# Performance work log

Measured on AMD Instinct MI355X. Metric: run time of the kernel, lower is better.

## Reference

```python
import jax, jax.numpy as jnp
import numpy as np

IN_SIZE = 4096   # input_size
OUT_SIZE = 4096  # output_size
RANK = 1024      # len(S_4), multiple of 32
GROUPSIZE = 128
BITS = 4
PACK = 32 // BITS  # 8 nibbles per int32
MAXQ_MASK = (1 << BITS) - 1  # 15


def _dequant4(qweight, qzeros, scales, g_idx):
    """GPTQ 4-bit dequant. qweight: int32 [K//8, N]; qzeros: int32 [G, N//8];
    scales: [G, N]; g_idx: int32 [K]. Returns W [K, N] with
    W[k, n] = (int4[k, n] - (zero4[g_idx[k], n] + 1)) * scales[g_idx[k], n]."""
    shifts = (jnp.arange(PACK, dtype=jnp.int32) * BITS)
    K = qweight.shape[0] * PACK
    N = qweight.shape[1]
    # unpack along rows: [K//8, 8, N] -> [K, N]
    intw = ((qweight[:, None, :] >> shifts[None, :, None]) & MAXQ_MASK).reshape(K, N)
    # unpack along cols: [G, N//8, 8] -> [G, N]; pack() stored zeros-1, so add 1 back
    zeros = ((qzeros[:, :, None] >> shifts[None, None, :]) & MAXQ_MASK).reshape(qzeros.shape[0], N) + 1
    sc = scales[g_idx]            # [K, N]
    zr = zeros[g_idx].astype(scales.dtype)  # [K, N]
    return (intw.astype(scales.dtype) - zr) * sc


def setup_inputs() -> dict:
    key = jax.random.key(0)
    ks = jax.random.split(key, 9)
    qweight_V = jax.random.randint(ks[0], (IN_SIZE // PACK, RANK), 0, 2**31 - 1, dtype=jnp.int32)
    qzeros_V = jax.random.randint(ks[1], (IN_SIZE // GROUPSIZE, RANK // PACK), 0, 2**31 - 1, dtype=jnp.int32)
    scales_V = jax.random.uniform(ks[2], (IN_SIZE // GROUPSIZE, RANK), dtype=jnp.float32) * 0.01 + 1e-3
    g_idx_V = (jnp.arange(IN_SIZE, dtype=jnp.int32) // GROUPSIZE).astype(jnp.int32)
    qweight_U = jax.random.randint(ks[3], (RANK // PACK, OUT_SIZE), 0, 2**31 - 1, dtype=jnp.int32)
    qzeros_U = jax.random.randint(ks[4], (RANK // GROUPSIZE, OUT_SIZE // PACK), 0, 2**31 - 1, dtype=jnp.int32)
    scales_U = jax.random.uniform(ks[5], (RANK // GROUPSIZE, OUT_SIZE), dtype=jnp.float32) * 0.01 + 1e-3
    g_idx_U = (jnp.arange(RANK, dtype=jnp.int32) // GROUPSIZE).astype(jnp.int32)
    S = jax.random.uniform(ks[6], (RANK,), dtype=jnp.float32) + 0.1  # singular values
    x = jax.random.normal(ks[7], (4, 2048, IN_SIZE), dtype=jnp.float32)
    return {"x": x,
            "qweight_V": qweight_V, "qzeros_V": qzeros_V, "scales_V": scales_V, "g_idx_V": g_idx_V,
            "qweight_U": qweight_U, "qzeros_U": qzeros_U, "scales_U": scales_U, "g_idx_U": g_idx_U,
            "S": S}


def reference(x, qweight_V, qzeros_V, scales_V, g_idx_V,
              qweight_U, qzeros_U, scales_U, g_idx_U, S):
    # weight_V: dequantized [IN_SIZE, RANK]; weight_U: dequantized [RANK, OUT_SIZE]
    weight_V = _dequant4(qweight_V, qzeros_V, scales_V, g_idx_V)
    weight_U = _dequant4(qweight_U, qzeros_U, scales_U, g_idx_U)
    # forward returns (weight_V @ diag(S) @ weight_U).T  -> [OUT_SIZE, IN_SIZE]
    # (the x @ W_V @ diag(S) @ W_U activation path in the source is dead code
    #  w.r.t. the returned value)
    return ((weight_V * S[None, :]) @ weight_U).T
```

## Files before the change

kernel.cpp:

```cpp
#include <hip/hip_runtime.h>

typedef __attribute__((ext_vector_type(8))) short bf16x8;
typedef __attribute__((ext_vector_type(4))) float f32x4;

__device__ __forceinline__ short f2bf(float f) {
  unsigned u = __builtin_bit_cast(unsigned, f);
  u += 0x7fffu + ((u >> 16) & 1u);
  return (short)(u >> 16);
}


__global__ __launch_bounds__(256) void dequant_v(const int* __restrict__ qw,
                                                 const int* __restrict__ qz,
                                                 const float* __restrict__ sc,
                                                 const float* __restrict__ S,
                                                 short* __restrict__ P) {
  const int t  = blockIdx.x * 256 + threadIdx.x;
  const int r8 = t & 127;
  const int k  = t >> 7;
  const int g  = k >> 7;
  const int kw = k >> 3;
  const int sh = (k & 7) << 2;
  const int r0 = r8 << 3;
  const int zw = qz[(g << 7) + r8];
  const int*   wq  = qw + kw * 1024 + r0;
  const float* scp = sc + (g << 10) + r0;
  const float* sp  = S + r0;
  bf16x8 res;
#pragma unroll
  for (int i = 0; i < 8; ++i) {
    int q = (wq[i] >> sh) & 15;
    int z = ((zw >> (i << 2)) & 15) + 1;
    res[i] = f2bf((float)(q - z) * scp[i] * sp[i]);
  }
  *(bf16x8*)(P + (k << 10) + r0) = res;
}

__global__ __launch_bounds__(256) void dequant_u(const int* __restrict__ qw,
                                                 const int* __restrict__ qz,
                                                 const float* __restrict__ sc,
                                                 short* __restrict__ Qt) {
  const int t  = blockIdx.x * 256 + threadIdx.x;
  const int rw = t & 127;
  const int n  = t >> 7;
  const int g  = rw >> 4;
  const int w  = qw[(rw << 12) + n];
  const int zw = qz[(g << 9) + (n >> 3)];
  const int z  = ((zw >> ((n & 7) << 2)) & 15) + 1;
  const float s = sc[(g << 12) + n];
  bf16x8 res;
#pragma unroll
  for (int i = 0; i < 8; ++i) {
    int q = (w >> (i << 2)) & 15;
    res[i] = f2bf((float)(q - z) * s);
  }
  *(bf16x8*)(Qt + (n << 10) + (rw << 3)) = res;
}

#define GLL(g, l)                                                              \
  __builtin_amdgcn_global_load_lds(                                            \
      (const __attribute__((address_space(1))) void*)(g),                      \
      (__attribute__((address_space(3))) void*)(l), 16, 0, 0)

__global__ __launch_bounds__(512, 2) void gemm256(const short* __restrict__ P,
                                                  const short* __restrict__ Qt,
                                                  float* __restrict__ out) {
  __shared__ __align__(16) char lds[131072];
  const int tid  = threadIdx.x;
  const int lane = tid & 63;
  const int wid  = tid >> 6;
  const int wm   = wid >> 2;
  const int wn   = wid & 3;
  const int m0 = (blockIdx.x >> 4) << 8;
  const int n0 = (blockIdx.x & 15) << 8;

  const int srow = tid >> 3;
  const int scol = ((tid & 7) << 4) ^ ((srow & 7) << 4);
  const short* gA = P  + (m0 + srow) * 1024 + (scol >> 1);
  const short* gB = Qt + (n0 + srow) * 1024 + (scol >> 1);

#define STG(gp, roff, half, ktv) do {                                          \
    const short* s_ = (gp) + (half) * 131072 + ((ktv) << 6);                   \
    char* d_ = lds + (roff) + (half) * 16384 + (wid << 10);                    \
    GLL(s_, d_);                                                               \
    GLL(s_ + 65536, d_ + 8192);                                                \
  } while (0)

  const int arow_b = ((wm << 7) + (lane & 15)) << 7;
  const int brow_b = ((wn << 6) + (lane & 15)) << 7;
  const int klo  = (lane >> 4) << 4;
  const int swz  = (lane & 7) << 4;
  const int offk0 = klo ^ swz;
  const int offk1 = (klo | 64) ^ swz;

  f32x4 acc[8][4];
#pragma unroll
  for (int mi = 0; mi < 8; ++mi)
#pragma unroll
    for (int ni = 0; ni < 4; ++ni) acc[mi][ni] = f32x4{0.f, 0.f, 0.f, 0.f};

  bf16x8 ah[4][2], bh0[2][2], bh1[2][2];

  STG(gA, 0, 0, 0);
  STG(gA, 0, 1, 0);
  STG(gB, 32768, 0, 0);
  STG(gB, 32768, 1, 0);
  STG(gA, 65536, 0, 1);
  STG(gA, 65536, 1, 1);
  STG(gB, 65536 + 32768, 0, 1);
  STG(gB, 65536 + 32768, 1, 1);
  asm volatile("s_waitcnt vmcnt(8)" ::: "memory");
  __builtin_amdgcn_s_barrier();

  for (int kt = 0; kt < 16; ++kt) {
    const int curbuf = (kt & 1) << 16;
    const char* Ab = lds + curbuf;
    const char* Bb = Ab + 32768;

#pragma unroll
    for (int i = 0; i < 4; ++i) {
      ah[i][0] = *(const bf16x8*)(Ab + arow_b + i * 2048 + offk0);
      ah[i][1] = *(const bf16x8*)(Ab + arow_b + i * 2048 + offk1);
    }
#pragma unroll
    for (int j = 0; j < 2; ++j) {
      bh0[j][0] = *(const bf16x8*)(Bb + brow_b + j * 2048 + offk0);
      bh0[j][1] = *(const bf16x8*)(Bb + brow_b + j * 2048 + offk1);
    }
    asm volatile("s_waitcnt lgkmcnt(0)" ::: "memory");
    __builtin_amdgcn_sched_barrier(0);
    __builtin_amdgcn_s_setprio(1);
#pragma unroll
    for (int kk = 0; kk < 2; ++kk)
#pragma unroll
      for (int i = 0; i < 4; ++i)
#pragma unroll
        for (int j = 0; j < 2; ++j)
          acc[i][j] = __builtin_amdgcn_mfma_f32_16x16x32_bf16(
              ah[i][kk], bh0[j][kk], acc[i][j], 0, 0, 0);
    __builtin_amdgcn_s_setprio(0);
    __builtin_amdgcn_s_barrier();

#pragma unroll
    for (int j = 0; j < 2; ++j) {
      bh1[j][0] = *(const bf16x8*)(Bb + brow_b + 4096 + j * 2048 + offk0);
      bh1[j][1] = *(const bf16x8*)(Bb + brow_b + 4096 + j * 2048 + offk1);
    }
    asm volatile("s_waitcnt lgkmcnt(0)" ::: "memory");
    __builtin_amdgcn_sched_barrier(0);
    __builtin_amdgcn_s_setprio(1);
#pragma unroll
    for (int kk = 0; kk < 2; ++kk)
#pragma unroll
      for (int i = 0; i < 4; ++i)
#pragma unroll
        for (int j = 0; j < 2; ++j)
          acc[i][2 + j] = __builtin_amdgcn_mfma_f32_16x16x32_bf16(
              ah[i][kk], bh1[j][kk], acc[i][2 + j], 0, 0, 0);
    __builtin_amdgcn_s_setprio(0);
    __builtin_amdgcn_s_barrier();

#pragma unroll
    for (int i = 0; i < 4; ++i) {
      ah[i][0] = *(const bf16x8*)(Ab + arow_b + 8192 + i * 2048 + offk0);
      ah[i][1] = *(const bf16x8*)(Ab + arow_b + 8192 + i * 2048 + offk1);
    }
    if (kt < 14) {
      STG(gB, curbuf + 32768, 0, kt + 2);
      STG(gB, curbuf + 32768, 1, kt + 2);
    }
    asm volatile("s_waitcnt lgkmcnt(0)" ::: "memory");
    __builtin_amdgcn_sched_barrier(0);
    __builtin_amdgcn_s_setprio(1);
#pragma unroll
    for (int kk = 0; kk < 2; ++kk)
#pragma unroll
      for (int i = 0; i < 4; ++i)
#pragma unroll
        for (int j = 0; j < 2; ++j)
          acc[4 + i][2 + j] = __builtin_amdgcn_mfma_f32_16x16x32_bf16(
              ah[i][kk], bh1[j][kk], acc[4 + i][2 + j], 0, 0, 0);
    __builtin_amdgcn_s_setprio(0);
    __builtin_amdgcn_s_barrier();

    if (kt < 14) {
      STG(gA, curbuf, 0, kt + 2);
      STG(gA, curbuf, 1, kt + 2);
    }
    __builtin_amdgcn_s_setprio(1);
#pragma unroll
    for (int kk = 0; kk < 2; ++kk)
#pragma unroll
      for (int i = 0; i < 4; ++i)
#pragma unroll
        for (int j = 0; j < 2; ++j)
          acc[4 + i][j] = __builtin_amdgcn_mfma_f32_16x16x32_bf16(
              ah[i][kk], bh0[j][kk], acc[4 + i][j], 0, 0, 0);
    __builtin_amdgcn_s_setprio(0);
    if (kt == 14) asm volatile("s_waitcnt vmcnt(0)" ::: "memory");
    else          asm volatile("s_waitcnt vmcnt(8)" ::: "memory");
    __builtin_amdgcn_s_barrier();
  }

  const int mbase = m0 + (wm << 7) + ((lane >> 4) << 2);
  const int nbase = n0 + (wn << 6) + (lane & 15);
#pragma unroll
  for (int mi = 0; mi < 8; ++mi)
#pragma unroll
    for (int ni = 0; ni < 4; ++ni)
      *(f32x4*)(out + (size_t)(nbase + ni * 16) * 4096 + mbase + mi * 16) =
          acc[mi][ni];
#undef STG
}

extern "C" void kernel_launch(void* const* d_in, const int* in_sizes, int n_in,
                              void* d_out, int out_size, void* d_ws, size_t ws_size,
                              hipStream_t stream) {
  const int*   qw_V = (const int*)d_in[1];
  const int*   qz_V = (const int*)d_in[2];
  const float* sc_V = (const float*)d_in[3];
  const int*   qw_U = (const int*)d_in[5];
  const int*   qz_U = (const int*)d_in[6];
  const float* sc_U = (const float*)d_in[7];
  const float* S    = (const float*)d_in[9];

  short* P  = (short*)d_ws;
  short* Qt = (short*)d_ws + 4096 * 1024;
  float* out = (float*)d_out;

  dequant_v<<<2048, 256, 0, stream>>>(qw_V, qz_V, sc_V, S, P);
  dequant_u<<<2048, 256, 0, stream>>>(qw_U, qz_U, sc_U, Qt);
  gemm256<<<256, 512, 0, stream>>>(P, Qt, out);
}
```

Measured before the change: 55.05 us.

## Pre-tile dequantized operands into MFMA fragment order for contiguous LDS staging

The dequant kernels now write A and B in a tile-major layout that matches the per-lane MFMA fragment order, so each 256x64 K-tile is a contiguous 32KB chunk. The GEMM stages it with contiguous global_load_lds copies and reads LDS at lane-linear offsets, dropping the XOR swizzle and per-row address math. The aim is fully coalesced global loads and conflict-free LDS reads. In exchange, the dequant kernels' reads are less coalesced, especially the V weight gathers.

```diff
diff --git a/kernel.cpp b/kernel.cpp
--- a/kernel.cpp
+++ b/kernel.cpp
@@ -14,47 +14,55 @@
                                                  const int* __restrict__ qz,
                                                  const float* __restrict__ sc,
                                                  const float* __restrict__ S,
-                                                 short* __restrict__ P) {
-  const int t  = blockIdx.x * 256 + threadIdx.x;
-  const int r8 = t & 127;
-  const int k  = t >> 7;
-  const int g  = k >> 7;
-  const int kw = k >> 3;
-  const int sh = (k & 7) << 2;
-  const int r0 = r8 << 3;
-  const int zw = qz[(g << 7) + r8];
-  const int*   wq  = qw + kw * 1024 + r0;
+                                                 short* __restrict__ A) {
+  const int t    = blockIdx.x * 256 + threadIdx.x;
+  const int tile = t >> 11;
+  const int blk  = (t >> 6) & 31;
+  const int lane = t & 63;
+  const int panel = tile >> 4, kt = tile & 15;
+  const int m  = (panel << 8) + (((blk >> 4) & 1) << 7) + (((blk >> 1) & 7) << 4) + (lane & 15);
+  const int r0 = (kt << 6) + ((blk & 1) << 5) + ((lane >> 4) << 3);
+
+  const int g  = m >> 7;
+  const int sh = (m & 7) << 2;
+  const int zw = qz[(g << 7) + (r0 >> 3)];
+  const int*   wq  = qw + (m >> 3) * 1024 + r0;
   const float* scp = sc + (g << 10) + r0;
   const float* sp  = S + r0;
   bf16x8 res;
 #pragma unroll
-  for (int i = 0; i < 8; ++i) {
-    int q = (wq[i] >> sh) & 15;
-    int z = ((zw >> (i << 2)) & 15) + 1;
-    res[i] = f2bf((float)(q - z) * scp[i] * sp[i]);
+  for (int e = 0; e < 8; ++e) {
+    int q = (wq[e] >> sh) & 15;
+    int z = ((zw >> (e << 2)) & 15) + 1;
+    res[e] = f2bf((float)(q - z) * scp[e] * sp[e]);
   }
-  *(bf16x8*)(P + (k << 10) + r0) = res;
+  *(bf16x8*)(A + ((size_t)t << 3)) = res;
 }
 
 __global__ __launch_bounds__(256) void dequant_u(const int* __restrict__ qw,
                                                  const int* __restrict__ qz,
                                                  const float* __restrict__ sc,
-                                                 short* __restrict__ Qt) {
-  const int t  = blockIdx.x * 256 + threadIdx.x;
-  const int rw = t & 127;
-  const int n  = t >> 7;
-  const int g  = rw >> 4;
-  const int w  = qw[(rw << 12) + n];
+                                                 short* __restrict__ B) {
+  const int t    = blockIdx.x * 256 + threadIdx.x;
+  const int tile = t >> 11;
+  const int blk  = (t >> 6) & 31;
+  const int lane = t & 63;
+  const int panel = tile >> 4, kt = tile & 15;
+  const int n  = (panel << 8) + (((blk >> 3) & 3) << 6) + (((blk >> 1) & 3) << 4) + (lane & 15);
+  const int r0 = (kt << 6) + ((blk & 1) << 5) + ((lane >> 4) << 3);
+
+  const int w  = qw[(r0 >> 3) * 4096 + n];
+  const int g  = r0 >> 7;
   const int zw = qz[(g << 9) + (n >> 3)];
   const int z  = ((zw >> ((n & 7) << 2)) & 15) + 1;
   const float s = sc[(g << 12) + n];
   bf16x8 res;
 #pragma unroll
-  for (int i = 0; i < 8; ++i) {
-    int q = (w >> (i << 2)) & 15;
-    res[i] = f2bf((float)(q - z) * s);
+  for (int e = 0; e < 8; ++e) {
+    int q = (w >> (e << 2)) & 15;
+    res[e] = f2bf((float)(q - z) * s);
   }
-  *(bf16x8*)(Qt + (n << 10) + (rw << 3)) = res;
+  *(bf16x8*)(B + ((size_t)t << 3)) = res;
 }
 
 #define GLL(g, l)                                                              \
@@ -62,8 +70,8 @@
       (const __attribute__((address_space(1))) void*)(g),                      \
       (__attribute__((address_space(3))) void*)(l), 16, 0, 0)
 
-__global__ __launch_bounds__(512, 2) void gemm256(const short* __restrict__ P,
-                                                  const short* __restrict__ Qt,
+__global__ __launch_bounds__(512, 2) void gemm256(const short* __restrict__ A,
+                                                  const short* __restrict__ B,
                                                   float* __restrict__ out) {
   __shared__ __align__(16) char lds[131072];
   const int tid  = threadIdx.x;
@@ -71,27 +79,31 @@
   const int wid  = tid >> 6;
   const int wm   = wid >> 2;
   const int wn   = wid & 3;
-  const int m0 = (blockIdx.x >> 4) << 8;
-  const int n0 = (blockIdx.x & 15) << 8;
-
-  const int srow = tid >> 3;
-  const int scol = ((tid & 7) << 4) ^ ((srow & 7) << 4);
-  const short* gA = P  + (m0 + srow) * 1024 + (scol >> 1);
-  const short* gB = Qt + (n0 + srow) * 1024 + (scol >> 1);
-
-#define STG(gp, roff, half, ktv) do {                                          \
-    const short* s_ = (gp) + (half) * 131072 + ((ktv) << 6);                   \
-    char* d_ = lds + (roff) + (half) * 16384 + (wid << 10);                    \
-    GLL(s_, d_);                                                               \
-    GLL(s_ + 65536, d_ + 8192);                                                \
+  const int mp = blockIdx.x >> 4;
+  const int np = blockIdx.x & 15;
+
+  const short* gA = A + ((size_t)(mp * 16) << 14) + (wid << 11) + (lane << 3);
+  const short* gB = B + ((size_t)(np * 16) << 14) + (wid << 11) + (lane << 3);
+
+#define STGA(buf, ktv) do {                                                    \
+    const short* s_ = gA + ((ktv) << 14);                                      \
+    char* d_ = lds + (buf) + (wid << 12);                                      \
+    GLL(s_,        d_);                                                        \
+    GLL(s_ +  512, d_ + 1024);                                                 \
+    GLL(s_ + 1024, d_ + 2048);                                                 \
+    GLL(s_ + 1536, d_ + 3072);                                                 \
   } while (0)
-
-  const int arow_b = ((wm << 7) + (lane & 15)) << 7;
-  const int brow_b = ((wn << 6) + (lane & 15)) << 7;
-  const int klo  = (lane >> 4) << 4;
-  const int swz  = (lane & 7) << 4;
-  const int offk0 = klo ^ swz;
-  const int offk1 = (klo | 64) ^ swz;
+#define STGB(buf, ktv) do {                                                    \
+    const short* s_ = gB + ((ktv) << 14);                                      \
+    char* d_ = lds + (buf) + 32768 + (wid << 12);                              \
+    GLL(s_,        d_);                                                        \
+    GLL(s_ +  512, d_ + 1024);                                                 \
+    GLL(s_ + 1024, d_ + 2048);                                                 \
+    GLL(s_ + 1536, d_ + 3072);                                                 \
+  } while (0)
+
+  const char* Ard = lds + (wm << 14) + (lane << 4);
+  const char* Brd = lds + 32768 + (wn << 13) + (lane << 4);
 
   f32x4 acc[8][4];
 #pragma unroll
@@ -101,31 +113,25 @@
 
   bf16x8 ah[4][2], bh0[2][2], bh1[2][2];
 
-  STG(gA, 0, 0, 0);
-  STG(gA, 0, 1, 0);
-  STG(gB, 32768, 0, 0);
-  STG(gB, 32768, 1, 0);
-  STG(gA, 65536, 0, 1);
-  STG(gA, 65536, 1, 1);
-  STG(gB, 65536 + 32768, 0, 1);
-  STG(gB, 65536 + 32768, 1, 1);
+  STGB(0, 0);
+  STGA(0, 0);
+  STGB(65536, 1);
+  STGA(65536, 1);
   asm volatile("s_waitcnt vmcnt(8)" ::: "memory");
   __builtin_amdgcn_s_barrier();
 
   for (int kt = 0; kt < 16; ++kt) {
     const int curbuf = (kt & 1) << 16;
-    const char* Ab = lds + curbuf;
-    const char* Bb = Ab + 32768;
 
 #pragma unroll
     for (int i = 0; i < 4; ++i) {
-      ah[i][0] = *(const bf16x8*)(Ab + arow_b + i * 2048 + offk0);
-      ah[i][1] = *(const bf16x8*)(Ab + arow_b + i * 2048 + offk1);
+      ah[i][0] = *(const bf16x8*)(Ard + curbuf + (i << 11));
+      ah[i][1] = *(const bf16x8*)(Ard + curbuf + (i << 11) + 1024);
     }
 #pragma unroll
     for (int j = 0; j < 2; ++j) {
-      bh0[j][0] = *(const bf16x8*)(Bb + brow_b + j * 2048 + offk0);
-      bh0[j][1] = *(const bf16x8*)(Bb + brow_b + j * 2048 + offk1);
+      bh0[j][0] = *(const bf16x8*)(Brd + curbuf + (j << 11));
+      bh0[j][1] = *(const bf16x8*)(Brd + curbuf + (j << 11) + 1024);
     }
     asm volatile("s_waitcnt lgkmcnt(0)" ::: "memory");
     __builtin_amdgcn_sched_barrier(0);
@@ -143,8 +149,8 @@
 
 #pragma unroll
     for (int j = 0; j < 2; ++j) {
-      bh1[j][0] = *(const bf16x8*)(Bb + brow_b + 4096 + j * 2048 + offk0);
-      bh1[j][1] = *(const bf16x8*)(Bb + brow_b + 4096 + j * 2048 + offk1);
+      bh1[j][0] = *(const bf16x8*)(Brd + curbuf + 4096 + (j << 11));
+      bh1[j][1] = *(const bf16x8*)(Brd + curbuf + 4096 + (j << 11) + 1024);
     }
     asm volatile("s_waitcnt lgkmcnt(0)" ::: "memory");
     __builtin_amdgcn_sched_barrier(0);
@@ -162,13 +168,10 @@
 
 #pragma unroll
     for (int i = 0; i < 4; ++i) {
-      ah[i][0] = *(const bf16x8*)(Ab + arow_b + 8192 + i * 2048 + offk0);
-      ah[i][1] = *(const bf16x8*)(Ab + arow_b + 8192 + i * 2048 + offk1);
-    }
-    if (kt < 14) {
-      STG(gB, curbuf + 32768, 0, kt + 2);
-      STG(gB, curbuf + 32768, 1, kt + 2);
-    }
+      ah[i][0] = *(const bf16x8*)(Ard + curbuf + 8192 + (i << 11));
+      ah[i][1] = *(const bf16x8*)(Ard + curbuf + 8192 + (i << 11) + 1024);
+    }
+    if (kt < 14) STGB(curbuf, kt + 2);
     asm volatile("s_waitcnt lgkmcnt(0)" ::: "memory");
     __builtin_amdgcn_sched_barrier(0);
     __builtin_amdgcn_s_setprio(1);
@@ -183,10 +186,7 @@
     __builtin_amdgcn_s_setprio(0);
     __builtin_amdgcn_s_barrier();
 
-    if (kt < 14) {
-      STG(gA, curbuf, 0, kt + 2);
-      STG(gA, curbuf, 1, kt + 2);
-    }
+    if (kt < 14) STGA(curbuf, kt + 2);
     __builtin_amdgcn_s_setprio(1);
 #pragma unroll
     for (int kk = 0; kk < 2; ++kk)
@@ -202,15 +202,16 @@
     __builtin_amdgcn_s_barrier();
   }
 
-  const int mbase = m0 + (wm << 7) + ((lane >> 4) << 2);
-  const int nbase = n0 + (wn << 6) + (lane & 15);
+  const int mbase = (mp << 8) + (wm << 7) + ((lane >> 4) << 2);
+  const int nbase = (np << 8) + (wn << 6) + (lane & 15);
 #pragma unroll
   for (int mi = 0; mi < 8; ++mi)
 #pragma unroll
     for (int ni = 0; ni < 4; ++ni)
       *(f32x4*)(out + (size_t)(nbase + ni * 16) * 4096 + mbase + mi * 16) =
           acc[mi][ni];
-#undef STG
+#undef STGA
+#undef STGB
 }
 
 extern "C" void kernel_launch(void* const* d_in, const int* in_sizes, int n_in,
@@ -224,11 +225,11 @@
   const float* sc_U = (const float*)d_in[7];
   const float* S    = (const float*)d_in[9];
 
-  short* P  = (short*)d_ws;
-  short* Qt = (short*)d_ws + 4096 * 1024;
+  short* A = (short*)d_ws;
+  short* B = (short*)d_ws + 4096 * 1024;
   float* out = (float*)d_out;
 
-  dequant_v<<<2048, 256, 0, stream>>>(qw_V, qz_V, sc_V, S, P);
-  dequant_u<<<2048, 256, 0, stream>>>(qw_U, qz_U, sc_U, Qt);
-  gemm256<<<256, 512, 0, stream>>>(P, Qt, out);
-}
+  dequant_v<<<2048, 256, 0, stream>>>(qw_V, qz_V, sc_V, S, A);
+  dequant_u<<<2048, 256, 0, stream>>>(qw_U, qz_U, sc_U, B);
+  gemm256<<<256, 512, 0, stream>>>(A, B, out);
+}
```

Measured after the change: 51.44 us. 1.07x faster.
